# Kernel tuning notes

Measured on AMD Instinct MI355X. Metric: run time of the kernel, lower is better.

The kernel has to match this reference:

```python
import jax, jax.numpy as jnp
import numpy as np

B, N = 256, 65536


def setup_inputs() -> dict:
    key = jax.random.key(0)
    k1, k2, k3 = jax.random.split(key, 3)
    src = jax.random.normal(k1, (B, 3, N), dtype=jnp.float32)
    tgt = jax.random.normal(k2, (B, 3, N), dtype=jnp.float32)
    weight = jax.random.uniform(k3, (B, N), dtype=jnp.float32)
    return {"src": src, "tgt": tgt, "weight": weight}


def reference(src, tgt, weight):
    # src, tgt: (B, 3, N); weight: (B, N)
    src_mean = src.mean(axis=2, keepdims=True)          # (B, 3, 1) -- unweighted, as in original
    tgt_mean = tgt.mean(axis=2, keepdims=True)
    src_c = src - src_mean
    tgt_c = tgt - tgt_mean
    # Weighted cross-covariance H = (src_c * w) @ tgt_c^T : (B, 3, 3)
    H = jnp.einsum('bin,bjn->bij', src_c * weight[:, None, :], tgt_c)
    # Batched tiny SVD (torch.svd returns V, jnp returns Vh)
    U, S, Vh = jnp.linalg.svd(H)
    V = jnp.swapaxes(Vh, -1, -2)
    Ut = jnp.swapaxes(U, -1, -2)
    R0 = V @ Ut                                          # (B, 3, 3)
    det = jnp.linalg.det(R0)                             # (B,)
    # Reflection fix: if det < 0, flip the last column of V (multiply by diag(1,1,-1))
    flip = jnp.where((det < 0)[:, None, None] & (jnp.arange(3) == 2)[None, None, :],
                     jnp.float32(-1.0), jnp.float32(1.0))
    R = (V * flip) @ Ut                                  # proper rotation, det=+1
    t = -R @ src_mean + tgt_mean                         # (B, 3, 1)
    Rt = jnp.swapaxes(R, -1, -2)                         # R <- R^T (as in original)
    t_out = -(Rt @ t)                                    # (B, 3, 1)
    return Rt, t_out.reshape(src.shape[0], 3)
```

## Files before the change

### kernel.cpp

```cpp
#include <hip/hip_runtime.h>

#define BATCH 256
#define NPTS 65536
#define NT 1024
#define NWAVES (NT / 64)

__global__ __launch_bounds__(NT, 1) void svdhead_reduce(
    const float* __restrict__ src, const float* __restrict__ tgt,
    const float* __restrict__ weight, float* __restrict__ ws)
{
    const int b   = blockIdx.x;
    const int tid = threadIdx.x;
    const int NV  = NPTS / 4;

    const float4* sp = (const float4*)(src + (size_t)b * 3 * NPTS);
    const float4* tp = (const float4*)(tgt + (size_t)b * 3 * NPTS);
    const float4* wp = (const float4*)(weight + (size_t)b * NPTS);

    float acc[22];
#pragma unroll
    for (int i = 0; i < 22; i++) acc[i] = 0.f;

    for (int k = tid; k < NV; k += NT) {
        float4 w4 = wp[k];
        float4 s0 = sp[k];
        float4 s1 = sp[k + NV];
        float4 s2 = sp[k + 2 * NV];
        float4 t0 = tp[k];
        float4 t1 = tp[k + NV];
        float4 t2 = tp[k + 2 * NV];
#define ACC1(C) do {                                                    \
        float wv = w4.C;                                                \
        float a0 = s0.C, a1 = s1.C, a2 = s2.C;                          \
        float c0 = t0.C, c1 = t1.C, c2 = t2.C;                          \
        acc[0] += a0;  acc[1] += a1;  acc[2] += a2;                     \
        acc[3] += c0;  acc[4] += c1;  acc[5] += c2;                     \
        acc[6] += wv;                                                   \
        float wa0 = wv * a0, wa1 = wv * a1, wa2 = wv * a2;              \
        acc[7]  += wa0; acc[8]  += wa1; acc[9]  += wa2;                 \
        acc[10] += wv * c0; acc[11] += wv * c1; acc[12] += wv * c2;     \
        acc[13] += wa0 * c0; acc[14] += wa0 * c1; acc[15] += wa0 * c2;  \
        acc[16] += wa1 * c0; acc[17] += wa1 * c1; acc[18] += wa1 * c2;  \
        acc[19] += wa2 * c0; acc[20] += wa2 * c1; acc[21] += wa2 * c2;  \
    } while (0)
        ACC1(x); ACC1(y); ACC1(z); ACC1(w);
#undef ACC1
    }

#pragma unroll
    for (int off = 32; off > 0; off >>= 1) {
#pragma unroll
        for (int i = 0; i < 22; i++) acc[i] += __shfl_down(acc[i], off, 64);
    }

    __shared__ float red[NWAVES][22];
    const int wave = tid >> 6;
    const int lane = tid & 63;
    if (lane == 0) {
#pragma unroll
        for (int i = 0; i < 22; i++) red[wave][i] = acc[i];
    }
    __syncthreads();

    if (tid < 22) {
        float s = 0.f;
#pragma unroll
        for (int wv = 0; wv < NWAVES; wv++) s += red[wv][tid];
        ws[(size_t)b * 22 + tid] = s;
    }
}

__global__ __launch_bounds__(256, 1) void svdhead_solve(
    const float* __restrict__ ws, float* __restrict__ out)
{
    const int b = blockIdx.x * blockDim.x + threadIdx.x;
    if (b >= BATCH) return;

    double S[22];
#pragma unroll
    for (int i = 0; i < 22; i++) S[i] = (double)ws[(size_t)b * 22 + i];

    const double invN = 1.0 / (double)NPTS;
    double ms[3] = { S[0] * invN, S[1] * invN, S[2] * invN };
    double mt[3] = { S[3] * invN, S[4] * invN, S[5] * invN };
    const double sw = S[6];

    double H[3][3];
    for (int i = 0; i < 3; i++)
        for (int j = 0; j < 3; j++)
            H[i][j] = S[13 + i * 3 + j] - ms[i] * S[10 + j] - mt[j] * S[7 + i]
                      + ms[i] * mt[j] * sw;

    double A[3][3];
    for (int i = 0; i < 3; i++)
        for (int j = 0; j < 3; j++) {
            double s = 0.0;
            for (int k = 0; k < 3; k++) s += H[k][i] * H[k][j];
            A[i][j] = s;
        }

    double V[3][3] = { {1,0,0}, {0,1,0}, {0,0,1} };
    for (int sweep = 0; sweep < 30; sweep++) {
        double off  = fabs(A[0][1]) + fabs(A[0][2]) + fabs(A[1][2]);
        double diag = fabs(A[0][0]) + fabs(A[1][1]) + fabs(A[2][2]);
        if (off <= 1e-13 * diag || off == 0.0) break;
        for (int p = 0; p < 2; p++)
            for (int q = p + 1; q < 3; q++) {
                double apq = A[p][q];
                if (fabs(apq) < 1e-300) continue;
                double tau = (A[q][q] - A[p][p]) / (2.0 * apq);
                double t = (tau >= 0.0 ? 1.0 : -1.0) / (fabs(tau) + sqrt(1.0 + tau * tau));
                double c = 1.0 / sqrt(1.0 + t * t);
                double s_ = t * c;
                for (int k = 0; k < 3; k++) {
                    double akp = A[k][p], akq = A[k][q];
                    A[k][p] = c * akp - s_ * akq;
                    A[k][q] = s_ * akp + c * akq;
                }
                for (int k = 0; k < 3; k++) {
                    double apk = A[p][k], aqk = A[q][k];
                    A[p][k] = c * apk - s_ * aqk;
                    A[q][k] = s_ * apk + c * aqk;
                }
                for (int k = 0; k < 3; k++) {
                    double vkp = V[k][p], vkq = V[k][q];
                    V[k][p] = c * vkp - s_ * vkq;
                    V[k][q] = s_ * vkp + c * vkq;
                }
            }
    }

    double lam[3] = { A[0][0], A[1][1], A[2][2] };
    int id[3] = { 0, 1, 2 };
    if (lam[id[0]] < lam[id[1]]) { int t = id[0]; id[0] = id[1]; id[1] = t; }
    if (lam[id[0]] < lam[id[2]]) { int t = id[0]; id[0] = id[2]; id[2] = t; }
    if (lam[id[1]] < lam[id[2]]) { int t = id[1]; id[1] = id[2]; id[2] = t; }
    double Vs[3][3];
    for (int k = 0; k < 3; k++)
        for (int i = 0; i < 3; i++) Vs[i][k] = V[i][id[k]];

    double U[3][3], sig[3];
    for (int k = 0; k < 3; k++) {
        double u0 = H[0][0] * Vs[0][k] + H[0][1] * Vs[1][k] + H[0][2] * Vs[2][k];
        double u1 = H[1][0] * Vs[0][k] + H[1][1] * Vs[1][k] + H[1][2] * Vs[2][k];
        double u2 = H[2][0] * Vs[0][k] + H[2][1] * Vs[1][k] + H[2][2] * Vs[2][k];
        sig[k] = sqrt(u0 * u0 + u1 * u1 + u2 * u2);
        U[0][k] = u0; U[1][k] = u1; U[2][k] = u2;
    }
    double smax = (sig[0] > 1e-300) ? sig[0] : 1e-300;

    if (sig[0] > 0.0) {
        U[0][0] /= sig[0]; U[1][0] /= sig[0]; U[2][0] /= sig[0];
    } else {
        U[0][0] = 1; U[1][0] = 0; U[2][0] = 0;
    }
    if (sig[1] > 1e-12 * smax) {
        U[0][1] /= sig[1]; U[1][1] /= sig[1]; U[2][1] /= sig[1];
    } else {
        double ax = fabs(U[0][0]), ay = fabs(U[1][0]), az = fabs(U[2][0]);
        double e0, e1, e2;
        if (ax <= ay && ax <= az)      { e0 = 1; e1 = 0; e2 = 0; }
        else if (ay <= az)             { e0 = 0; e1 = 1; e2 = 0; }
        else                           { e0 = 0; e1 = 0; e2 = 1; }
        double cx = U[1][0] * e2 - U[2][0] * e1;
        double cy = U[2][0] * e0 - U[0][0] * e2;
        double cz = U[0][0] * e1 - U[1][0] * e0;
        double n = sqrt(cx * cx + cy * cy + cz * cz);
        U[0][1] = cx / n; U[1][1] = cy / n; U[2][1] = cz / n;
    }
    if (sig[2] > 1e-12 * smax) {
        U[0][2] /= sig[2]; U[1][2] /= sig[2]; U[2][2] /= sig[2];
    } else {
        U[0][2] = U[1][0] * U[2][1] - U[2][0] * U[1][1];
        U[1][2] = U[2][0] * U[0][1] - U[0][0] * U[2][1];
        U[2][2] = U[0][0] * U[1][1] - U[1][0] * U[0][1];
    }

    double detH = H[0][0] * (H[1][1] * H[2][2] - H[1][2] * H[2][1])
                - H[0][1] * (H[1][0] * H[2][2] - H[1][2] * H[2][0])
                + H[0][2] * (H[1][0] * H[2][1] - H[1][1] * H[2][0]);
    double d2 = (detH < 0.0) ? -1.0 : 1.0;

    double R[3][3];
    for (int i = 0; i < 3; i++)
        for (int j = 0; j < 3; j++)
            R[i][j] = Vs[i][0] * U[j][0] + Vs[i][1] * U[j][1] + d2 * Vs[i][2] * U[j][2];

    double tv[3];
    for (int i = 0; i < 3; i++)
        tv[i] = mt[i] - (R[i][0] * ms[0] + R[i][1] * ms[1] + R[i][2] * ms[2]);
    double to[3];
    for (int i = 0; i < 3; i++)
        to[i] = -(R[0][i] * tv[0] + R[1][i] * tv[1] + R[2][i] * tv[2]);

    float* outR = out + (size_t)b * 9;
    for (int i = 0; i < 3; i++)
        for (int j = 0; j < 3; j++)
            outR[i * 3 + j] = (float)R[j][i];
    float* outT = out + (size_t)BATCH * 9 + (size_t)b * 3;
    for (int i = 0; i < 3; i++) outT[i] = (float)to[i];
}

extern "C" void kernel_launch(void* const* d_in, const int* in_sizes, int n_in,
                              void* d_out, int out_size, void* d_ws, size_t ws_size,
                              hipStream_t stream)
{
    const float* src    = (const float*)d_in[0];
    const float* tgt    = (const float*)d_in[1];
    const float* weight = (const float*)d_in[2];
    float* out = (float*)d_out;
    float* ws  = (float*)d_ws;

    svdhead_reduce<<<BATCH, NT, 0, stream>>>(src, tgt, weight, ws);
    svdhead_solve<<<1, 256, 0, stream>>>(ws, out);
}
```

Baseline: 437.8 us.

## Split per-batch reduction across multiple blocks and parallelize solve per batch

The reduction kernel now splits each batch's points across 8 blocks of 256 threads, writing partial sums that the solve kernel combines. The loop has a fixed trip count with unroll 2 to expose more memory-level parallelism. The solve kernel runs one block per batch, summing the partials in double before a single thread does the 3x3 SVD. This aims to improve bandwidth utilization and load balance, at the cost of extra workspace traffic and a second-stage combine.

```diff
diff --git a/kernel.cpp b/kernel.cpp
--- a/kernel.cpp
+++ b/kernel.cpp
@@ -2,16 +2,20 @@
 
 #define BATCH 256
 #define NPTS 65536
-#define NT 1024
+#define NT 256
+#define SPLIT 8
 #define NWAVES (NT / 64)
-
-__global__ __launch_bounds__(NT, 1) void svdhead_reduce(
+#define CHUNKS_PER_BLOCK (NPTS / 4 / SPLIT)
+#define ITERS (CHUNKS_PER_BLOCK / NT)
+
+__global__ __launch_bounds__(NT, 4) void svdhead_reduce(
     const float* __restrict__ src, const float* __restrict__ tgt,
     const float* __restrict__ weight, float* __restrict__ ws)
 {
-    const int b   = blockIdx.x;
-    const int tid = threadIdx.x;
-    const int NV  = NPTS / 4;
+    const int b    = blockIdx.x / SPLIT;
+    const int part = blockIdx.x % SPLIT;
+    const int tid  = threadIdx.x;
+    const int NV   = NPTS / 4;
 
     const float4* sp = (const float4*)(src + (size_t)b * 3 * NPTS);
     const float4* tp = (const float4*)(tgt + (size_t)b * 3 * NPTS);
@@ -21,7 +25,11 @@
 #pragma unroll
     for (int i = 0; i < 22; i++) acc[i] = 0.f;
 
-    for (int k = tid; k < NV; k += NT) {
+    const int base = part * CHUNKS_PER_BLOCK + tid;
+
+#pragma unroll 2
+    for (int it = 0; it < ITERS; it++) {
+        const int k = base + it * NT;
         float4 w4 = wp[k];
         float4 s0 = sp[k];
         float4 s1 = sp[k + NV];
@@ -66,19 +74,26 @@
         float s = 0.f;
 #pragma unroll
         for (int wv = 0; wv < NWAVES; wv++) s += red[wv][tid];
-        ws[(size_t)b * 22 + tid] = s;
+        ws[((size_t)b * SPLIT + part) * 22 + tid] = s;
     }
 }
 
-__global__ __launch_bounds__(256, 1) void svdhead_solve(
+__global__ __launch_bounds__(64, 1) void svdhead_solve(
     const float* __restrict__ ws, float* __restrict__ out)
 {
-    const int b = blockIdx.x * blockDim.x + threadIdx.x;
-    if (b >= BATCH) return;
-
-    double S[22];
-#pragma unroll
-    for (int i = 0; i < 22; i++) S[i] = (double)ws[(size_t)b * 22 + i];
+    const int b   = blockIdx.x;
+    const int tid = threadIdx.x;
+
+    __shared__ double S[22];
+    if (tid < 22) {
+        double s = 0.0;
+#pragma unroll
+        for (int p = 0; p < SPLIT; p++)
+            s += (double)ws[((size_t)b * SPLIT + p) * 22 + tid];
+        S[tid] = s;
+    }
+    __syncthreads();
+    if (tid != 0) return;
 
     const double invN = 1.0 / (double)NPTS;
     double ms[3] = { S[0] * invN, S[1] * invN, S[2] * invN };
@@ -211,6 +226,6 @@
     float* out = (float*)d_out;
     float* ws  = (float*)d_ws;
 
-    svdhead_reduce<<<BATCH, NT, 0, stream>>>(src, tgt, weight, ws);
-    svdhead_solve<<<1, 256, 0, stream>>>(ws, out);
+    svdhead_reduce<<<BATCH * SPLIT, NT, 0, stream>>>(src, tgt, weight, ws);
+    svdhead_solve<<<BATCH, 64, 0, stream>>>(ws, out);
 }
```

After: 435.6 us. Within noise of the previous version (-0.5%).
